# Optimization experiments

Hardware: AMD Instinct MI355X
Metric: run time of the kernel (lower is better)

## Reference

```python
import jax, jax.numpy as jnp
import numpy as np

N = 50000      # nodes
E = 800000     # edges (avg degree 16)
F_IN = 256     # num_node_features
H = 256        # hidden_dim
L = 2          # num_message_passing_rounds - 1 hidden conv layers


def setup_inputs() -> dict:
    key = jax.random.key(0)
    ks = jax.random.split(key, 8)
    x = jax.random.normal(ks[0], (N, F_IN), dtype=jnp.float32)
    edge_index = jax.random.randint(ks[1], (2, E), 0, N, dtype=jnp.int32)
    init = lambda k, shape, fan: jax.random.normal(k, shape, dtype=jnp.float32) / np.float32(np.sqrt(fan))
    WA_in = init(ks[2], (F_IN, H), F_IN)   # proj_in.A weight (stored [in,out])
    WB_in = init(ks[3], (F_IN, H), F_IN)   # proj_in.B weight
    A_stack = init(ks[4], (L, H, H), H)    # conv layers' A weights
    B_stack = init(ks[5], (L, H, H), H)    # conv layers' B weights
    W_out = init(ks[6], (H, 1), H)         # proj_out weight
    b_out = jnp.zeros((1,), jnp.float32)   # proj_out bias
    return {"x": x, "edge_index": edge_index, "WA_in": WA_in, "WB_in": WB_in,
            "A_stack": A_stack, "B_stack": B_stack, "W_out": W_out, "b_out": b_out}


def reference(x, edge_index, WA_in, WB_in, A_stack, B_stack, W_out, b_out):
    src, dst = edge_index[0], edge_index[1]
    # in-degree per node; PyG scatter-mean divides by max(deg, 1)
    deg = jax.ops.segment_sum(jnp.ones((E,), x.dtype), dst, num_segments=N)
    inv_deg = (1.0 / jnp.maximum(deg, 1.0))[:, None]  # [N,1]

    def mean_agg(h):
        # gather x_j = h[src], scatter-mean into dst -> [N, d]
        return jax.ops.segment_sum(h[src], dst, num_segments=N) * inv_deg

    # proj_in: A(mean_msg) + B(x)
    h = mean_agg(x) @ WA_in + x @ WB_in
    # hidden conv rounds with sigmoid (use_relu=False)
    for i in range(L):
        h = jax.nn.sigmoid(mean_agg(h) @ A_stack[i] + h @ B_stack[i])
    # proj_out + squeeze (output_logits=True)
    return (h @ W_out + b_out).squeeze()  # [N]
```

## Files before the change

### kernel.cpp

```cpp
#include <hip/hip_runtime.h>

typedef unsigned short u16;
typedef unsigned int u32;
typedef __attribute__((ext_vector_type(8))) short short8;
typedef __attribute__((ext_vector_type(4))) float f32x4;
typedef __attribute__((ext_vector_type(2))) float f32x2;

__device__ __forceinline__ float bf2f(u16 u) {
    return __uint_as_float(((u32)u) << 16);
}
__device__ __forceinline__ u16 f2bf(float f) {
    u32 u = __float_as_uint(f);
    u += 0x7fff + ((u >> 16) & 1);
    return (u16)(u >> 16);
}
__device__ __forceinline__ u32 pack2(float a, float b) {
    return (u32)f2bf(a) | ((u32)f2bf(b) << 16);
}
__device__ __forceinline__ u32 pk_fp8x4(float f0, float f1, float f2, float f3) {
    int w = __builtin_amdgcn_cvt_pk_fp8_f32(f0, f1, 0, false);
    w = __builtin_amdgcn_cvt_pk_fp8_f32(f2, f3, w, true);
    return (u32)w;
}
__device__ __forceinline__ void acc4(float* a, u32 w) {
    f32x2 lo = __builtin_amdgcn_cvt_pk_f32_fp8((int)w, false);
    f32x2 hi = __builtin_amdgcn_cvt_pk_f32_fp8((int)w, true);
    a[0] += lo.x; a[1] += lo.y; a[2] += hi.x; a[3] += hi.y;
}
__device__ __forceinline__ void acc4m(float* a, u32 w, float m) {
    f32x2 lo = __builtin_amdgcn_cvt_pk_f32_fp8((int)w, false);
    f32x2 hi = __builtin_amdgcn_cvt_pk_f32_fp8((int)w, true);
    a[0] += m * lo.x; a[1] += m * lo.y; a[2] += m * hi.x; a[3] += m * hi.y;
}
__device__ __forceinline__ void acc16(float* a, uint4 v) {
    acc4(a + 0, v.x); acc4(a + 4, v.y); acc4(a + 8, v.z); acc4(a + 12, v.w);
}
__device__ __forceinline__ void acc16m(float* a, uint4 v, float m) {
    acc4m(a + 0, v.x, m); acc4m(a + 4, v.y, m); acc4m(a + 8, v.z, m); acc4m(a + 12, v.w, m);
}


__global__ void cvt_x_kernel(const float* __restrict__ x, u16* __restrict__ xb,
                             u32* __restrict__ xq, int n) {
    int i = blockIdx.x * 256 + threadIdx.x;
    int row = i >> 6;
    ushort4 o;
    u32 q;
    if (row < n) {
        float4 v = ((const float4*)x)[i];
        o.x = f2bf(v.x); o.y = f2bf(v.y); o.z = f2bf(v.z); o.w = f2bf(v.w);
        q = pk_fp8x4(v.x, v.y, v.z, v.w);
    } else {
        o.x = o.y = o.z = o.w = 0;
        q = 0;
    }
    ((ushort4*)xb)[i] = o;
    xq[i] = q;
}

__global__ void cvt_w_kernel(const float* __restrict__ WA, const float* __restrict__ WB,
                             const float* __restrict__ As, const float* __restrict__ Bs,
                             u16* __restrict__ wT, int nlayers) {
    int i = blockIdx.x * 256 + threadIdx.x;
    const int per = 256 * 512;
    if (i >= nlayers * per) return;
    int l = i / per;
    int rem = i - l * per;
    int nn = rem >> 9;
    int k = rem & 511;
    const float* Aw = (l == 0) ? WA : As + (size_t)(l - 1) * 65536;
    const float* Bw = (l == 0) ? WB : Bs + (size_t)(l - 1) * 65536;
    float v = (k < 256) ? Aw[(size_t)k * 256 + nn] : Bw[(size_t)(k - 256) * 256 + nn];
    wT[i] = f2bf(v);
}


__global__ __launch_bounds__(256) void hist_kernel(const int* __restrict__ dst,
                                                   int* __restrict__ ccnt, int e, int nb) {
    __shared__ int h[256];
    int tid = threadIdx.x;
    h[tid] = 0;
    __syncthreads();
    int e0 = blockIdx.x * 4096;
#pragma unroll
    for (int j = 0; j < 16; ++j) {
        int i = e0 + j * 256 + tid;
        if (i < e) atomicAdd(&h[dst[i] >> 8], 1);
    }
    __syncthreads();
    if (tid < nb) {
        int v = h[tid];
        if (v) atomicAdd(&ccnt[tid], v);
    }
}

__global__ __launch_bounds__(256) void scan_coarse_kernel(const int* __restrict__ ccnt,
                                                          int* __restrict__ cbase,
                                                          int* __restrict__ rowptr,
                                                          int nb, int n, int e) {
    __shared__ int sh[256];
    int t = threadIdx.x;
    int v = (t < nb) ? ccnt[t] : 0;
    int x = v;
    sh[t] = x; __syncthreads();
    for (int o = 1; o < 256; o <<= 1) {
        int y = (t >= o) ? sh[t - o] : 0;
        __syncthreads();
        x += y; sh[t] = x; __syncthreads();
    }
    if (t < nb) cbase[t] = x - v;
    if (t == 0) { cbase[nb] = e; rowptr[n] = e; }
}

__global__ __launch_bounds__(256) void passA_kernel(const int* __restrict__ src,
                                                    const int* __restrict__ dst,
                                                    const int* __restrict__ cbase,
                                                    int* __restrict__ cfill,
                                                    u32* __restrict__ tmp, int e, int nb) {
    __shared__ int ph[256], pb[256], pr[256], cb[256];
    __shared__ u32 ed[4096];
    int tid = threadIdx.x;
    ph[tid] = 0; pr[tid] = 0;
    cb[tid] = (tid < nb) ? cbase[tid] : 0;
    __syncthreads();
    int e0 = blockIdx.x * 4096;
#pragma unroll
    for (int j = 0; j < 16; ++j) {
        int i = e0 + j * 256 + tid;
        u32 p = 0xFFFFFFFFu;
        if (i < e) {
            int d = dst[i];
            p = ((u32)d << 16) | (u32)src[i];
            atomicAdd(&ph[d >> 8], 1);
        }
        ed[j * 256 + tid] = p;
    }
    __syncthreads();
    pb[tid] = (tid < nb && ph[tid]) ? atomicAdd(&cfill[tid], ph[tid]) : 0;
    __syncthreads();
#pragma unroll
    for (int j = 0; j < 16; ++j) {
        u32 p = ed[j * 256 + tid];
        if (p != 0xFFFFFFFFu) {
            int bk = p >> 24;
            int r = atomicAdd(&pr[bk], 1);
            tmp[cb[bk] + pb[bk] + r] = p;
        }
    }
}

__global__ __launch_bounds__(256) void passB_kernel(const u32* __restrict__ tmp,
                                                    const int* __restrict__ cbase,
                                                    int* __restrict__ rowptr,
                                                    float* __restrict__ invd,
                                                    int* __restrict__ srcs, int n) {
    __shared__ int h[256], loc[256], cnt2[256], sh[256];
    int b = blockIdx.x;
    int tid = threadIdx.x;
    int base = cbase[b];
    int cnt = cbase[b + 1] - base;
    int node0 = b << 8;
    h[tid] = 0; cnt2[tid] = 0;
    __syncthreads();
    for (int i = tid; i < cnt; i += 256)
        atomicAdd(&h[(tmp[base + i] >> 16) & 255], 1);
    __syncthreads();
    int c = h[tid];
    int x = c;
    sh[tid] = x; __syncthreads();
    for (int o = 1; o < 256; o <<= 1) {
        int y = (tid >= o) ? sh[tid - o] : 0;
        __syncthreads();
        x += y; sh[tid] = x; __syncthreads();
    }
    loc[tid] = x - c;
    int node = node0 + tid;
    if (node < n) {
        rowptr[node] = base + x - c;
        invd[node] = 1.0f / (float)(c > 0 ? c : 1);
    }
    __syncthreads();
    for (int i = tid; i < cnt; i += 256) {
        u32 p = tmp[base + i];
        int ln = (p >> 16) & 255;
        int r = atomicAdd(&cnt2[ln], 1);
        srcs[base + loc[ln] + r] = (int)(p & 0xffffu);
    }
}


__global__ __launch_bounds__(256) void agg_kernel(const unsigned char* __restrict__ q,
                                                  u16* __restrict__ mb,
                                                  const int* __restrict__ rowptr,
                                                  const int* __restrict__ srcs,
                                                  const float* __restrict__ invd,
                                                  int n, int npad) {
    int gw = (blockIdx.x * 256 + threadIdx.x) >> 6;
    int lane = threadIdx.x & 63;
    int qd = lane >> 4;
    int fl = lane & 15;
    if (gw >= npad) return;
    u16* orow = mb + (size_t)gw * 256;
    if (gw >= n) {
        if (lane < 16) {
            uint4 z; z.x = z.y = z.z = z.w = 0;
            uint4* p = (uint4*)(orow + lane * 16);
            p[0] = z; p[1] = z;
        }
        return;
    }
    int beg = rowptr[gw], end = rowptr[gw + 1];
    float a[16];
#pragma unroll
    for (int i = 0; i < 16; ++i) a[i] = 0.f;
    for (int base = beg; base < end; base += 64) {
        int cnt = end - base;
        if (cnt > 64) cnt = 64;
        int el = (lane < cnt) ? srcs[base + lane] : 0;
        int t = 0;
        for (; 4 * t + 8 <= cnt; t += 2) {
            int s0 = __shfl(el, 4 * t + qd);
            int s1 = __shfl(el, 4 * t + 4 + qd);
            uint4 v0 = *(const uint4*)(q + (size_t)s0 * 256 + fl * 16);
            uint4 v1 = *(const uint4*)(q + (size_t)s1 * 256 + fl * 16);
            acc16(a, v0);
            acc16(a, v1);
        }
        for (; 4 * t < cnt; ++t) {
            int ei = 4 * t + qd;
            int sj = __shfl(el, ei & 63);
            float m = (ei < cnt) ? 1.0f : 0.0f;
            uint4 v = *(const uint4*)(q + (size_t)sj * 256 + fl * 16);
            acc16m(a, v, m);
        }
    }
#pragma unroll
    for (int i = 0; i < 16; ++i) {
        a[i] += __shfl_xor(a[i], 16);
        a[i] += __shfl_xor(a[i], 32);
    }
    if (lane < 16) {
        float sc = invd[gw];
        uint4 o0, o1;
        o0.x = pack2(a[0] * sc, a[1] * sc);
        o0.y = pack2(a[2] * sc, a[3] * sc);
        o0.z = pack2(a[4] * sc, a[5] * sc);
        o0.w = pack2(a[6] * sc, a[7] * sc);
        o1.x = pack2(a[8] * sc, a[9] * sc);
        o1.y = pack2(a[10] * sc, a[11] * sc);
        o1.z = pack2(a[12] * sc, a[13] * sc);
        o1.w = pack2(a[14] * sc, a[15] * sc);
        uint4* p = (uint4*)(orow + lane * 16);
        p[0] = o0; p[1] = o1;
    }
}


__global__ __launch_bounds__(256, 2) void gemm_kernel(const u16* __restrict__ mA,
                                                      const u16* __restrict__ cur,
                                                      const u16* __restrict__ wT,
                                                      u16* __restrict__ outb,
                                                      unsigned char* __restrict__ hqb,
                                                      const float* __restrict__ wo,
                                                      const float* __restrict__ bo,
                                                      float* __restrict__ out,
                                                      int n, int apply_sigmoid, int fin) {
    __shared__ u16 lA[128 * 32];
    __shared__ u16 lB[256 * 32];
    __shared__ float lO[2][128];
    int r0 = blockIdx.x * 128;
    int tid = threadIdx.x;
    int lane = tid & 63;
    int w = tid >> 6;
    int wrow = w >> 1, wcol = w & 1;
    int lrow = lane & 15, quad = lane >> 4;

    f32x4 acc[4][8] = {};

    for (int ks = 0; ks < 16; ++ks) {
        int k0 = ks * 32;
        const u16* srcA = (k0 < 256) ? mA : cur;
        int kk = k0 & 255;
        __syncthreads();
#pragma unroll
        for (int p = 0; p < 2; ++p) {
            int li = p * 256 + tid;
            int row = li >> 2;
            int seg = (li & 3) << 3;
            const u16* gA = srcA + (size_t)(r0 + row) * 256 + kk + seg;
            __builtin_amdgcn_global_load_lds(
                (__attribute__((address_space(1))) u32*)(gA),
                (__attribute__((address_space(3))) u32*)(lA + (size_t)li * 8), 16, 0, 0);
        }
#pragma unroll
        for (int p = 0; p < 4; ++p) {
            int li = p * 256 + tid;
            int row = li >> 2;
            int seg = (li & 3) << 3;
            const u16* gB = wT + (size_t)row * 512 + k0 + seg;
            __builtin_amdgcn_global_load_lds(
                (__attribute__((address_space(1))) u32*)(gB),
                (__attribute__((address_space(3))) u32*)(lB + (size_t)li * 8), 16, 0, 0);
        }
        __syncthreads();

        short8 a[4], b[8];
#pragma unroll
        for (int t = 0; t < 4; ++t)
            a[t] = *(const short8*)(lA + ((size_t)(wrow * 64 + t * 16 + lrow) * 32 + quad * 8));
#pragma unroll
        for (int t = 0; t < 8; ++t)
            b[t] = *(const short8*)(lB + ((size_t)(wcol * 128 + t * 16 + lrow) * 32 + quad * 8));
#pragma unroll
        for (int rt = 0; rt < 4; ++rt)
#pragma unroll
            for (int ct = 0; ct < 8; ++ct)
                acc[rt][ct] = __builtin_amdgcn_mfma_f32_16x16x32_bf16(a[rt], b[ct], acc[rt][ct], 0, 0, 0);
    }

    if (!fin) {
#pragma unroll
        for (int rt = 0; rt < 4; ++rt) {
            int rbase = r0 + wrow * 64 + rt * 16 + quad * 4;
#pragma unroll
            for (int r = 0; r < 4; ++r) {
                int row = rbase + r;
                if (row < n) {
#pragma unroll
                    for (int ct = 0; ct < 8; ++ct) {
                        float v = acc[rt][ct][r];
                        if (apply_sigmoid) v = 1.0f / (1.0f + __expf(-v));
                        int col = wcol * 128 + ct * 16 + lrow;
                        outb[(size_t)row * 256 + col] = f2bf(v);
                        u32 wq = (u32)__builtin_amdgcn_cvt_pk_fp8_f32(v, v, 0, false);
                        hqb[(size_t)row * 256 + col] = (unsigned char)(wq & 0xff);
                    }
                }
            }
        }
    } else {
        float wv[8];
#pragma unroll
        for (int ct = 0; ct < 8; ++ct) wv[ct] = wo[wcol * 128 + ct * 16 + lrow];
#pragma unroll
        for (int rt = 0; rt < 4; ++rt) {
#pragma unroll
            for (int r = 0; r < 4; ++r) {
                float s = 0.f;
#pragma unroll
                for (int ct = 0; ct < 8; ++ct) {
                    float v = acc[rt][ct][r];
                    v = 1.0f / (1.0f + __expf(-v));
                    s += v * wv[ct];
                }
                s += __shfl_xor(s, 1);
                s += __shfl_xor(s, 2);
                s += __shfl_xor(s, 4);
                s += __shfl_xor(s, 8);
                if (lrow == 0) {
                    int rowlocal = wrow * 64 + rt * 16 + quad * 4 + r;
                    lO[wcol][rowlocal] = s;
                }
            }
        }
        __syncthreads();
        if (tid < 128) {
            int row = r0 + tid;
            if (row < n) out[row] = lO[0][tid] + lO[1][tid] + bo[0];
        }
    }
}


extern "C" void kernel_launch(void* const* d_in, const int* in_sizes, int n_in,
                              void* d_out, int out_size, void* d_ws, size_t ws_size,
                              hipStream_t stream) {
    const float* x  = (const float*)d_in[0];
    const int*   ei = (const int*)d_in[1];
    const float* WA = (const float*)d_in[2];
    const float* WB = (const float*)d_in[3];
    const float* As = (const float*)d_in[4];
    const float* Bs = (const float*)d_in[5];
    const float* Wo = (const float*)d_in[6];
    const float* bo = (const float*)d_in[7];
    float* out = (float*)d_out;

    const int H = 256;
    int N = in_sizes[0] / H;
    int E = in_sizes[1] / 2;
    int L = in_sizes[4] / (H * H);
    int NPAD = (N + 127) & ~127;
    int NB = (N + 255) >> 8;

    char* wsp = (char*)d_ws;
    size_t off = 0;
    auto alloc = [&](size_t b) { size_t o = off; off += (b + 255) & ~(size_t)255; return o; };
    int*   rowptr = (int*)(wsp + alloc((size_t)(NPAD + 1) * 4));
    int*   ccnt   = (int*)(wsp + alloc(1024));
    int*   cbase  = (int*)(wsp + alloc(1032 + 256));
    int*   cfill  = (int*)(wsp + alloc(1024));
    float* invd   = (float*)(wsp + alloc((size_t)NPAD * 4));
    int*   srcs   = (int*)(wsp + alloc((size_t)E * 4));
    u16*   xb     = (u16*)(wsp + alloc((size_t)NPAD * H * 2));
    u16*   hbuf   = (u16*)(wsp + alloc((size_t)NPAD * H * 2));
    u16*   mb     = (u16*)(wsp + alloc((size_t)NPAD * H * 2));
    u32*   xq     = (u32*)(wsp + alloc((size_t)NPAD * H));
    u32*   hq     = (u32*)(wsp + alloc((size_t)NPAD * H));
    u16*   wT     = (u16*)(wsp + alloc((size_t)(L + 1) * 512 * 256 * 2));
    u32*   tmp    = (u32*)mb;

    const int* esrc = ei;
    const int* edst = ei + E;

    hipMemsetAsync(ccnt, 0, 1024, stream);
    hipMemsetAsync(cfill, 0, 1024, stream);

    int gridE = (E + 4095) / 4096;
    cvt_x_kernel<<<NPAD / 4, 256, 0, stream>>>(x, xb, xq, N);
    cvt_w_kernel<<<((L + 1) * 512 * 256 + 255) / 256, 256, 0, stream>>>(WA, WB, As, Bs, wT, L + 1);
    hist_kernel<<<gridE, 256, 0, stream>>>(edst, ccnt, E, NB);
    scan_coarse_kernel<<<1, 256, 0, stream>>>(ccnt, cbase, rowptr, NB, N, E);
    passA_kernel<<<gridE, 256, 0, stream>>>(esrc, edst, cbase, cfill, tmp, E, NB);
    passB_kernel<<<NB, 256, 0, stream>>>(tmp, cbase, rowptr, invd, srcs, N);

    const u16* cur = xb;
    const unsigned char* curq = (const unsigned char*)xq;
    for (int s = 0; s <= L; ++s) {
        int fin = (s == L) ? 1 : 0;
        agg_kernel<<<NPAD / 4, 256, 0, stream>>>(curq, mb, rowptr, srcs, invd, N, NPAD);
        gemm_kernel<<<NPAD / 128, 256, 0, stream>>>(mb, cur, wT + (size_t)s * 512 * 256, hbuf,
                                                    (unsigned char*)hq, Wo, bo, out, N,
                                                    s > 0 ? 1 : 0, fin);
        if (!fin) {
            cur = hbuf;
            curq = (const unsigned char*)hq;
        }
    }
}
```

Before: 335.9 us.

## Fuse neighbor aggregation into GEMM tile and merge prep kernels

Each 64-row GEMM block now gathers and mean-aggregates its own nodes' fp8 neighbor features straight into LDS, then runs the MFMA GEMM reading the aggregated half of K from LDS. This removes the separate aggregation kernel and the bf16 round trip through global memory for the message buffer. The fp8 output buffer is ping-ponged so neighbor reads never race with writes from other blocks. The input conversion, weight conversion and histogram kernels are also merged into one launch. The costs are smaller GEMM tiles, which reload the weights twice as often, and lower occupancy for the latency-bound gather because of the larger LDS footprint.

```diff
diff --git a/kernel.cpp b/kernel.cpp
--- a/kernel.cpp
+++ b/kernel.cpp
@@ -40,59 +40,63 @@
 }
 
 
-__global__ void cvt_x_kernel(const float* __restrict__ x, u16* __restrict__ xb,
-                             u32* __restrict__ xq, int n) {
-    int i = blockIdx.x * 256 + threadIdx.x;
-    int row = i >> 6;
-    ushort4 o;
-    u32 q;
-    if (row < n) {
-        float4 v = ((const float4*)x)[i];
-        o.x = f2bf(v.x); o.y = f2bf(v.y); o.z = f2bf(v.z); o.w = f2bf(v.w);
-        q = pk_fp8x4(v.x, v.y, v.z, v.w);
-    } else {
-        o.x = o.y = o.z = o.w = 0;
-        q = 0;
-    }
-    ((ushort4*)xb)[i] = o;
-    xq[i] = q;
-}
-
-__global__ void cvt_w_kernel(const float* __restrict__ WA, const float* __restrict__ WB,
-                             const float* __restrict__ As, const float* __restrict__ Bs,
-                             u16* __restrict__ wT, int nlayers) {
-    int i = blockIdx.x * 256 + threadIdx.x;
-    const int per = 256 * 512;
-    if (i >= nlayers * per) return;
-    int l = i / per;
-    int rem = i - l * per;
-    int nn = rem >> 9;
-    int k = rem & 511;
-    const float* Aw = (l == 0) ? WA : As + (size_t)(l - 1) * 65536;
-    const float* Bw = (l == 0) ? WB : Bs + (size_t)(l - 1) * 65536;
-    float v = (k < 256) ? Aw[(size_t)k * 256 + nn] : Bw[(size_t)(k - 256) * 256 + nn];
-    wT[i] = f2bf(v);
-}
-
-
-__global__ __launch_bounds__(256) void hist_kernel(const int* __restrict__ dst,
+__global__ __launch_bounds__(256) void prep_kernel(const float* __restrict__ x,
+                                                   u16* __restrict__ xb, u32* __restrict__ xq,
+                                                   int n, int nx,
+                                                   const float* __restrict__ WA,
+                                                   const float* __restrict__ WB,
+                                                   const float* __restrict__ As,
+                                                   const float* __restrict__ Bs,
+                                                   u16* __restrict__ wT, int nlayers, int nw,
+                                                   const int* __restrict__ dst,
                                                    int* __restrict__ ccnt, int e, int nb) {
     __shared__ int h[256];
+    int b = blockIdx.x;
     int tid = threadIdx.x;
-    h[tid] = 0;
-    __syncthreads();
-    int e0 = blockIdx.x * 4096;
-#pragma unroll
-    for (int j = 0; j < 16; ++j) {
-        int i = e0 + j * 256 + tid;
-        if (i < e) atomicAdd(&h[dst[i] >> 8], 1);
-    }
-    __syncthreads();
-    if (tid < nb) {
-        int v = h[tid];
-        if (v) atomicAdd(&ccnt[tid], v);
-    }
-}
+    if (b < nx) {
+        int i = b * 256 + tid;
+        int row = i >> 6;
+        ushort4 o;
+        u32 q;
+        if (row < n) {
+            float4 v = ((const float4*)x)[i];
+            o.x = f2bf(v.x); o.y = f2bf(v.y); o.z = f2bf(v.z); o.w = f2bf(v.w);
+            q = pk_fp8x4(v.x, v.y, v.z, v.w);
+        } else {
+            o.x = o.y = o.z = o.w = 0;
+            q = 0;
+        }
+        ((ushort4*)xb)[i] = o;
+        xq[i] = q;
+    } else if (b < nx + nw) {
+        int i = (b - nx) * 256 + tid;
+        const int per = 256 * 512;
+        if (i >= nlayers * per) return;
+        int l = i / per;
+        int rem = i - l * per;
+        int nn = rem >> 9;
+        int k = rem & 511;
+        const float* Aw = (l == 0) ? WA : As + (size_t)(l - 1) * 65536;
+        const float* Bw = (l == 0) ? WB : Bs + (size_t)(l - 1) * 65536;
+        float v = (k < 256) ? Aw[(size_t)k * 256 + nn] : Bw[(size_t)(k - 256) * 256 + nn];
+        wT[i] = f2bf(v);
+    } else {
+        h[tid] = 0;
+        __syncthreads();
+        int e0 = (b - nx - nw) * 4096;
+#pragma unroll
+        for (int j = 0; j < 16; ++j) {
+            int i = e0 + j * 256 + tid;
+            if (i < e) atomicAdd(&h[dst[i] >> 8], 1);
+        }
+        __syncthreads();
+        if (tid < nb) {
+            int v = h[tid];
+            if (v) atomicAdd(&ccnt[tid], v);
+        }
+    }
+}
+
 
 __global__ __launch_bounds__(256) void scan_coarse_kernel(const int* __restrict__ ccnt,
                                                           int* __restrict__ cbase,
@@ -189,109 +193,91 @@
 }
 
 
-__global__ __launch_bounds__(256) void agg_kernel(const unsigned char* __restrict__ q,
-                                                  u16* __restrict__ mb,
-                                                  const int* __restrict__ rowptr,
-                                                  const int* __restrict__ srcs,
-                                                  const float* __restrict__ invd,
-                                                  int n, int npad) {
-    int gw = (blockIdx.x * 256 + threadIdx.x) >> 6;
-    int lane = threadIdx.x & 63;
-    int qd = lane >> 4;
-    int fl = lane & 15;
-    if (gw >= npad) return;
-    u16* orow = mb + (size_t)gw * 256;
-    if (gw >= n) {
-        if (lane < 16) {
-            uint4 z; z.x = z.y = z.z = z.w = 0;
-            uint4* p = (uint4*)(orow + lane * 16);
-            p[0] = z; p[1] = z;
-        }
-        return;
-    }
-    int beg = rowptr[gw], end = rowptr[gw + 1];
-    float a[16];
-#pragma unroll
-    for (int i = 0; i < 16; ++i) a[i] = 0.f;
-    for (int base = beg; base < end; base += 64) {
-        int cnt = end - base;
-        if (cnt > 64) cnt = 64;
-        int el = (lane < cnt) ? srcs[base + lane] : 0;
-        int t = 0;
-        for (; 4 * t + 8 <= cnt; t += 2) {
-            int s0 = __shfl(el, 4 * t + qd);
-            int s1 = __shfl(el, 4 * t + 4 + qd);
-            uint4 v0 = *(const uint4*)(q + (size_t)s0 * 256 + fl * 16);
-            uint4 v1 = *(const uint4*)(q + (size_t)s1 * 256 + fl * 16);
-            acc16(a, v0);
-            acc16(a, v1);
-        }
-        for (; 4 * t < cnt; ++t) {
-            int ei = 4 * t + qd;
-            int sj = __shfl(el, ei & 63);
-            float m = (ei < cnt) ? 1.0f : 0.0f;
-            uint4 v = *(const uint4*)(q + (size_t)sj * 256 + fl * 16);
-            acc16m(a, v, m);
-        }
-    }
-#pragma unroll
-    for (int i = 0; i < 16; ++i) {
-        a[i] += __shfl_xor(a[i], 16);
-        a[i] += __shfl_xor(a[i], 32);
-    }
-    if (lane < 16) {
-        float sc = invd[gw];
-        uint4 o0, o1;
-        o0.x = pack2(a[0] * sc, a[1] * sc);
-        o0.y = pack2(a[2] * sc, a[3] * sc);
-        o0.z = pack2(a[4] * sc, a[5] * sc);
-        o0.w = pack2(a[6] * sc, a[7] * sc);
-        o1.x = pack2(a[8] * sc, a[9] * sc);
-        o1.y = pack2(a[10] * sc, a[11] * sc);
-        o1.z = pack2(a[12] * sc, a[13] * sc);
-        o1.w = pack2(a[14] * sc, a[15] * sc);
-        uint4* p = (uint4*)(orow + lane * 16);
-        p[0] = o0; p[1] = o1;
-    }
-}
-
-
-__global__ __launch_bounds__(256, 2) void gemm_kernel(const u16* __restrict__ mA,
-                                                      const u16* __restrict__ cur,
-                                                      const u16* __restrict__ wT,
-                                                      u16* __restrict__ outb,
-                                                      unsigned char* __restrict__ hqb,
-                                                      const float* __restrict__ wo,
-                                                      const float* __restrict__ bo,
-                                                      float* __restrict__ out,
-                                                      int n, int apply_sigmoid, int fin) {
-    __shared__ u16 lA[128 * 32];
+__global__ __launch_bounds__(256, 2) void fused_kernel(const unsigned char* __restrict__ q,
+                                                       const u16* __restrict__ cur,
+                                                       const u16* __restrict__ wT,
+                                                       const int* __restrict__ rowptr,
+                                                       const int* __restrict__ srcs,
+                                                       const float* __restrict__ invd,
+                                                       u16* __restrict__ outb,
+                                                       unsigned char* __restrict__ hqb,
+                                                       const float* __restrict__ wo,
+                                                       const float* __restrict__ bo,
+                                                       float* __restrict__ out,
+                                                       int n, int apply_sigmoid, int fin) {
+    __shared__ u16 lM[64 * 264];
+    __shared__ u16 lA[64 * 32];
     __shared__ u16 lB[256 * 32];
-    __shared__ float lO[2][128];
-    int r0 = blockIdx.x * 128;
+    __shared__ float lO[4][64];
+    int r0 = blockIdx.x * 64;
     int tid = threadIdx.x;
     int lane = tid & 63;
     int w = tid >> 6;
-    int wrow = w >> 1, wcol = w & 1;
     int lrow = lane & 15, quad = lane >> 4;
-
-    f32x4 acc[4][8] = {};
-
+    int qd = quad;
+    int fl = lrow;
+
+    for (int i = 0; i < 16; ++i) {
+        int nd = w * 16 + i;
+        int gw = r0 + nd;
+        if (gw >= n) {
+            if (lane < 16) {
+                uint4 z; z.x = z.y = z.z = z.w = 0;
+                *(uint4*)&lM[nd * 264 + fl * 16] = z;
+                *(uint4*)&lM[nd * 264 + fl * 16 + 8] = z;
+            }
+            continue;
+        }
+        int beg = rowptr[gw], end = rowptr[gw + 1];
+        float a[16];
+#pragma unroll
+        for (int t = 0; t < 16; ++t) a[t] = 0.f;
+        for (int base = beg; base < end; base += 64) {
+            int cnt = end - base;
+            if (cnt > 64) cnt = 64;
+            int el = (lane < cnt) ? srcs[base + lane] : 0;
+            int t = 0;
+            for (; 4 * t + 8 <= cnt; t += 2) {
+                int s0 = __shfl(el, 4 * t + qd);
+                int s1 = __shfl(el, 4 * t + 4 + qd);
+                uint4 v0 = *(const uint4*)(q + (size_t)s0 * 256 + fl * 16);
+                uint4 v1 = *(const uint4*)(q + (size_t)s1 * 256 + fl * 16);
+                acc16(a, v0);
+                acc16(a, v1);
+            }
+            for (; 4 * t < cnt; ++t) {
+                int ei = 4 * t + qd;
+                int sj = __shfl(el, ei & 63);
+                float m = (ei < cnt) ? 1.0f : 0.0f;
+                uint4 v = *(const uint4*)(q + (size_t)sj * 256 + fl * 16);
+                acc16m(a, v, m);
+            }
+        }
+#pragma unroll
+        for (int t = 0; t < 16; ++t) {
+            a[t] += __shfl_xor(a[t], 16);
+            a[t] += __shfl_xor(a[t], 32);
+        }
+        if (lane < 16) {
+            float sc = invd[gw];
+            uint4 o0, o1;
+            o0.x = pack2(a[0] * sc, a[1] * sc);
+            o0.y = pack2(a[2] * sc, a[3] * sc);
+            o0.z = pack2(a[4] * sc, a[5] * sc);
+            o0.w = pack2(a[6] * sc, a[7] * sc);
+            o1.x = pack2(a[8] * sc, a[9] * sc);
+            o1.y = pack2(a[10] * sc, a[11] * sc);
+            o1.z = pack2(a[12] * sc, a[13] * sc);
+            o1.w = pack2(a[14] * sc, a[15] * sc);
+            *(uint4*)&lM[nd * 264 + fl * 16] = o0;
+            *(uint4*)&lM[nd * 264 + fl * 16 + 8] = o1;
+        }
+    }
+
+    f32x4 acc[4][4] = {};
     for (int ks = 0; ks < 16; ++ks) {
         int k0 = ks * 32;
-        const u16* srcA = (k0 < 256) ? mA : cur;
-        int kk = k0 & 255;
-        __syncthreads();
-#pragma unroll
-        for (int p = 0; p < 2; ++p) {
-            int li = p * 256 + tid;
-            int row = li >> 2;
-            int seg = (li & 3) << 3;
-            const u16* gA = srcA + (size_t)(r0 + row) * 256 + kk + seg;
-            __builtin_amdgcn_global_load_lds(
-                (__attribute__((address_space(1))) u32*)(gA),
-                (__attribute__((address_space(3))) u32*)(lA + (size_t)li * 8), 16, 0, 0);
-        }
+        __syncthreads();
 #pragma unroll
         for (int p = 0; p < 4; ++p) {
             int li = p * 256 + tid;
@@ -302,35 +288,50 @@
                 (__attribute__((address_space(1))) u32*)(gB),
                 (__attribute__((address_space(3))) u32*)(lB + (size_t)li * 8), 16, 0, 0);
         }
-        __syncthreads();
-
-        short8 a[4], b[8];
+        if (ks >= 8) {
+            int li = tid;
+            int row = li >> 2;
+            int seg = (li & 3) << 3;
+            const u16* gA = cur + (size_t)(r0 + row) * 256 + (k0 & 255) + seg;
+            __builtin_amdgcn_global_load_lds(
+                (__attribute__((address_space(1))) u32*)(gA),
+                (__attribute__((address_space(3))) u32*)(lA + (size_t)li * 8), 16, 0, 0);
+        }
+        __syncthreads();
+
+        short8 a[4], b[4];
+        if (ks < 8) {
+#pragma unroll
+            for (int t = 0; t < 4; ++t)
+                a[t] = *(const short8*)&lM[(size_t)(t * 16 + lrow) * 264 + k0 + quad * 8];
+        } else {
+#pragma unroll
+            for (int t = 0; t < 4; ++t)
+                a[t] = *(const short8*)&lA[(size_t)(t * 16 + lrow) * 32 + quad * 8];
+        }
 #pragma unroll
         for (int t = 0; t < 4; ++t)
-            a[t] = *(const short8*)(lA + ((size_t)(wrow * 64 + t * 16 + lrow) * 32 + quad * 8));
-#pragma unroll
-        for (int t = 0; t < 8; ++t)
-            b[t] = *(const short8*)(lB + ((size_t)(wcol * 128 + t * 16 + lrow) * 32 + quad * 8));
+            b[t] = *(const short8*)&lB[(size_t)(w * 64 + t * 16 + lrow) * 32 + quad * 8];
 #pragma unroll
         for (int rt = 0; rt < 4; ++rt)
 #pragma unroll
-            for (int ct = 0; ct < 8; ++ct)
+            for (int ct = 0; ct < 4; ++ct)
                 acc[rt][ct] = __builtin_amdgcn_mfma_f32_16x16x32_bf16(a[rt], b[ct], acc[rt][ct], 0, 0, 0);
     }
 
     if (!fin) {
 #pragma unroll
         for (int rt = 0; rt < 4; ++rt) {
-            int rbase = r0 + wrow * 64 + rt * 16 + quad * 4;
+            int rbase = r0 + rt * 16 + quad * 4;
 #pragma unroll
             for (int r = 0; r < 4; ++r) {
                 int row = rbase + r;
                 if (row < n) {
 #pragma unroll
-                    for (int ct = 0; ct < 8; ++ct) {
+                    for (int ct = 0; ct < 4; ++ct) {
                         float v = acc[rt][ct][r];
                         if (apply_sigmoid) v = 1.0f / (1.0f + __expf(-v));
-                        int col = wcol * 128 + ct * 16 + lrow;
+                        int col = w * 64 + ct * 16 + lrow;
                         outb[(size_t)row * 256 + col] = f2bf(v);
                         u32 wq = (u32)__builtin_amdgcn_cvt_pk_fp8_f32(v, v, 0, false);
                         hqb[(size_t)row * 256 + col] = (unsigned char)(wq & 0xff);
@@ -339,16 +340,16 @@
             }
         }
     } else {
-        float wv[8];
-#pragma unroll
-        for (int ct = 0; ct < 8; ++ct) wv[ct] = wo[wcol * 128 + ct * 16 + lrow];
+        float wv[4];
+#pragma unroll
+        for (int ct = 0; ct < 4; ++ct) wv[ct] = wo[w * 64 + ct * 16 + lrow];
 #pragma unroll
         for (int rt = 0; rt < 4; ++rt) {
 #pragma unroll
             for (int r = 0; r < 4; ++r) {
                 float s = 0.f;
 #pragma unroll
-                for (int ct = 0; ct < 8; ++ct) {
+                for (int ct = 0; ct < 4; ++ct) {
                     float v = acc[rt][ct][r];
                     v = 1.0f / (1.0f + __expf(-v));
                     s += v * wv[ct];
@@ -358,15 +359,16 @@
                 s += __shfl_xor(s, 4);
                 s += __shfl_xor(s, 8);
                 if (lrow == 0) {
-                    int rowlocal = wrow * 64 + rt * 16 + quad * 4 + r;
-                    lO[wcol][rowlocal] = s;
+                    int rowlocal = rt * 16 + quad * 4 + r;
+                    lO[w][rowlocal] = s;
                 }
             }
         }
         __syncthreads();
-        if (tid < 128) {
+        if (tid < 64) {
             int row = r0 + tid;
-            if (row < n) out[row] = lO[0][tid] + lO[1][tid] + bo[0];
+            if (row < n)
+                out[row] = lO[0][tid] + lO[1][tid] + lO[2][tid] + lO[3][tid] + bo[0];
         }
     }
 }
@@ -396,44 +398,47 @@
     size_t off = 0;
     auto alloc = [&](size_t b) { size_t o = off; off += (b + 255) & ~(size_t)255; return o; };
     int*   rowptr = (int*)(wsp + alloc((size_t)(NPAD + 1) * 4));
-    int*   ccnt   = (int*)(wsp + alloc(1024));
+    int*   ccnt   = (int*)(wsp + alloc(2048));
+    int*   cfill  = ccnt + 256;
     int*   cbase  = (int*)(wsp + alloc(1032 + 256));
-    int*   cfill  = (int*)(wsp + alloc(1024));
     float* invd   = (float*)(wsp + alloc((size_t)NPAD * 4));
     int*   srcs   = (int*)(wsp + alloc((size_t)E * 4));
     u16*   xb     = (u16*)(wsp + alloc((size_t)NPAD * H * 2));
     u16*   hbuf   = (u16*)(wsp + alloc((size_t)NPAD * H * 2));
-    u16*   mb     = (u16*)(wsp + alloc((size_t)NPAD * H * 2));
     u32*   xq     = (u32*)(wsp + alloc((size_t)NPAD * H));
-    u32*   hq     = (u32*)(wsp + alloc((size_t)NPAD * H));
+    u32*   hq0    = (u32*)(wsp + alloc((size_t)NPAD * H));
+    u32*   hq1    = (u32*)(wsp + alloc((size_t)NPAD * H));
     u16*   wT     = (u16*)(wsp + alloc((size_t)(L + 1) * 512 * 256 * 2));
-    u32*   tmp    = (u32*)mb;
+    u32*   tmp    = (u32*)hbuf;
 
     const int* esrc = ei;
     const int* edst = ei + E;
 
-    hipMemsetAsync(ccnt, 0, 1024, stream);
-    hipMemsetAsync(cfill, 0, 1024, stream);
+    hipMemsetAsync(ccnt, 0, 2048, stream);
 
     int gridE = (E + 4095) / 4096;
-    cvt_x_kernel<<<NPAD / 4, 256, 0, stream>>>(x, xb, xq, N);
-    cvt_w_kernel<<<((L + 1) * 512 * 256 + 255) / 256, 256, 0, stream>>>(WA, WB, As, Bs, wT, L + 1);
-    hist_kernel<<<gridE, 256, 0, stream>>>(edst, ccnt, E, NB);
+    int nx = NPAD / 4;
+    int nw = ((L + 1) * 512 * 256 + 255) / 256;
+    prep_kernel<<<nx + nw + gridE, 256, 0, stream>>>(x, xb, xq, N, nx,
+                                                     WA, WB, As, Bs, wT, L + 1, nw,
+                                                     edst, ccnt, E, NB);
     scan_coarse_kernel<<<1, 256, 0, stream>>>(ccnt, cbase, rowptr, NB, N, E);
     passA_kernel<<<gridE, 256, 0, stream>>>(esrc, edst, cbase, cfill, tmp, E, NB);
     passB_kernel<<<NB, 256, 0, stream>>>(tmp, cbase, rowptr, invd, srcs, N);
 
     const u16* cur = xb;
     const unsigned char* curq = (const unsigned char*)xq;
+    u32* nextq = hq0;
     for (int s = 0; s <= L; ++s) {
         int fin = (s == L) ? 1 : 0;
-        agg_kernel<<<NPAD / 4, 256, 0, stream>>>(curq, mb, rowptr, srcs, invd, N, NPAD);
-        gemm_kernel<<<NPAD / 128, 256, 0, stream>>>(mb, cur, wT + (size_t)s * 512 * 256, hbuf,
-                                                    (unsigned char*)hq, Wo, bo, out, N,
+        fused_kernel<<<NPAD / 64, 256, 0, stream>>>(curq, cur, wT + (size_t)s * 512 * 256,
+                                                    rowptr, srcs, invd, hbuf,
+                                                    (unsigned char*)nextq, Wo, bo, out, N,
                                                     s > 0 ? 1 : 0, fin);
         if (!fin) {
             cur = hbuf;
-            curq = (const unsigned char*)hq;
-        }
-    }
-}
+            curq = (const unsigned char*)nextq;
+            nextq = (nextq == hq0) ? hq1 : hq0;
+        }
+    }
+}
```

Result: slower. 480.5 us (+43.0%).
